# Kernel tuning notes

Hardware: AMD Instinct MI355X
Metric: run time of the kernel (lower is better)

## Reference

```python
import jax, jax.numpy as jnp
import numpy as np

N, IN_F, OUT_F = 8192, 512, 256
NEG_INF = -9e15
LEAKY_SLOPE = 0.25


def setup_inputs() -> dict:
    key = jax.random.key(0)
    k1, k2, k3, k4, k5, k6 = jax.random.split(key, 6)
    inp = {
        "input": jax.random.normal(k1, (N, IN_F), dtype=jnp.float32),
        "adj": jax.random.randint(k2, (N, N), 0, 2, dtype=jnp.int32),
        # learned params (xavier-normal-ish scale)
        "weights": jax.random.normal(k3, (IN_F, OUT_F), dtype=jnp.float32) * (2.0 / (IN_F + OUT_F)) ** 0.5,
        "a1": jax.random.normal(k4, (OUT_F, 1), dtype=jnp.float32) * (2.0 / (OUT_F + 1)) ** 0.5,
        "a2": jax.random.normal(k5, (OUT_F, 1), dtype=jnp.float32) * (2.0 / (OUT_F + 1)) ** 0.5,
        "bias": jax.random.uniform(k6, (OUT_F,), dtype=jnp.float32, minval=-1.0 / OUT_F ** 0.5, maxval=1.0 / OUT_F ** 0.5),
    }
    return inp


def reference(input, adj, weights, a1, a2, bias):
    # h = input @ W  : [N, out]
    h = input @ weights
    # e[i,j] = leaky_relu((h@a1)[i] + (h@a2)[j])  : [N, N] via broadcast
    e1 = h @ a1  # [N,1]
    e2 = h @ a2  # [N,1]
    e = e1 + e2.T
    e = jnp.where(e > 0, e, LEAKY_SLOPE * e)
    # mask non-edges, row softmax (dropout omitted: deterministic reference)
    scores = jnp.where(adj > 0, e, NEG_INF)
    attention = jax.nn.softmax(scores, axis=1)
    # aggregate + bias
    return attention @ h + bias
```

## Files before the change

### kernel.cpp

```cpp
#include <hip/hip_runtime.h>
#include <hip/hip_fp16.h>

typedef __attribute__((ext_vector_type(8))) short short8;
typedef __attribute__((ext_vector_type(4))) float floatx4;
typedef __attribute__((ext_vector_type(4))) unsigned int uintx4;
typedef __attribute__((ext_vector_type(2))) unsigned int uintx2;
typedef __attribute__((ext_vector_type(4))) int intx4;
typedef __attribute__((ext_vector_type(4))) unsigned short ushortx4;
typedef unsigned int u32;

#define NN 8192
#define KIN 512
#define COUT 256
#define SHIFT 16.0f

__device__ __forceinline__ unsigned int f2bf(float f) {
  unsigned int u = __float_as_uint(f);
  return (u + 0x7FFFu + ((u >> 16) & 1u)) >> 16;
}

__device__ __forceinline__ u32 pkbf(float lo, float hi) {
  u32 a = __float_as_uint(lo) + 0x8000u;
  u32 b = __float_as_uint(hi) + 0x8000u;
  return __builtin_amdgcn_perm(b, a, 0x07060302u);
}

__device__ __forceinline__ short8 pack8(const float* p) {
  uintx4 w;
  w.x = pkbf(p[0], p[1]);
  w.y = pkbf(p[2], p[3]);
  w.z = pkbf(p[4], p[5]);
  w.w = pkbf(p[6], p[7]);
  union { uintx4 u; short8 s; } cv; cv.u = w;
  return cv.s;
}

__global__ __launch_bounds__(256)
void k_prep(const float* __restrict__ in, ushortx4* __restrict__ inA4,
            const float* __restrict__ w, unsigned short* __restrict__ wt) {
  int b = blockIdx.x;
  if (b < 4096) {
    int idx = b * 256 + threadIdx.x;
    floatx4 v = ((const floatx4*)in)[idx];
    ushortx4 o;
    o.x = (unsigned short)f2bf(v.x);
    o.y = (unsigned short)f2bf(v.y);
    o.z = (unsigned short)f2bf(v.z);
    o.w = (unsigned short)f2bf(v.w);
    inA4[idx] = o;
  } else {
    int idx = (b - 4096) * 256 + threadIdx.x;
    int k = idx >> 8, c = idx & 255;
    wt[c * KIN + k] = (unsigned short)f2bf(w[idx]);
  }
}

__global__ __launch_bounds__(256)
void k_gemm_h(const unsigned short* __restrict__ inA, const unsigned short* __restrict__ wt,
              const float* __restrict__ a1, const float* __restrict__ a2,
              unsigned short* __restrict__ ht, float* __restrict__ e1, float* __restrict__ e2,
              float* __restrict__ A1, float* __restrict__ A2, u32* __restrict__ e2pk) {
  int wave = threadIdx.x >> 6;
  int lane = threadIdx.x & 63;
  int n = lane & 15, q = lane >> 4;
  int row0 = blockIdx.x * 64 + wave * 16;
  int mrow = row0 + n;

  floatx4 acc[16];
#pragma unroll
  for (int t = 0; t < 16; ++t) acc[t] = (floatx4){0.f, 0.f, 0.f, 0.f};

  for (int kc = 0; kc < KIN / 32; ++kc) {
    int k0 = kc * 32 + q * 8;
    short8 a = *(const short8*)(inA + (size_t)mrow * KIN + k0);
#pragma unroll
    for (int nt = 0; nt < 16; ++nt) {
      short8 b = *(const short8*)(wt + (size_t)(nt * 16 + n) * KIN + k0);
      acc[nt] = __builtin_amdgcn_mfma_f32_16x16x32_bf16(a, b, acc[nt], 0, 0, 0);
    }
  }

  int i0 = row0 + q * 4;
#pragma unroll
  for (int nt = 0; nt < 16; ++nt) {
    int c = nt * 16 + n;
    uintx2 pk;
    pk.x = f2bf(acc[nt][0]) | (f2bf(acc[nt][1]) << 16);
    pk.y = f2bf(acc[nt][2]) | (f2bf(acc[nt][3]) << 16);
    *(uintx2*)(ht + (size_t)c * NN + i0) = pk;
  }

  float s1[4] = {0.f, 0.f, 0.f, 0.f}, s2[4] = {0.f, 0.f, 0.f, 0.f};
#pragma unroll
  for (int nt = 0; nt < 16; ++nt) {
    float w1 = a1[nt * 16 + n];
    float w2 = a2[nt * 16 + n];
#pragma unroll
    for (int r = 0; r < 4; ++r) {
      s1[r] += acc[nt][r] * w1;
      s2[r] += acc[nt][r] * w2;
    }
  }
#pragma unroll
  for (int m = 1; m < 16; m <<= 1) {
#pragma unroll
    for (int r = 0; r < 4; ++r) {
      s1[r] += __shfl_xor(s1[r], m);
      s2[r] += __shfl_xor(s2[r], m);
    }
  }
  if (n == 0) {
#pragma unroll
    for (int r = 0; r < 4; ++r) {
      float v1 = s1[r], v2 = s2[r];
      e1[i0 + r] = v1;
      e2[i0 + r] = v2;
      A1[i0 + r] = __expf(v1 - 8.0f);
      A2[i0 + r] = __expf(0.25f * v1 - 8.0f);
      u32 b1 = f2bf(__expf(v2 - 8.0f));
      u32 b2 = f2bf(__expf(0.25f * v2 - 8.0f));
      e2pk[i0 + r] = (b1 << 16) | b2;
    }
  }
}

__global__ __launch_bounds__(256, 2)
void k_attn_direct(const int* __restrict__ adj, const unsigned short* __restrict__ ht,
                   const float* __restrict__ A1, const float* __restrict__ A2,
                   const u32* __restrict__ e2pk,
                   __half2* __restrict__ oph, float* __restrict__ Dpart) {
  int b = blockIdx.x;
  int rg = b >> 3, js = b & 7;
  int wave = threadIdx.x >> 6, lane = threadIdx.x & 63;
  int n = lane & 15, q = lane >> 4;
  int rowbase = rg * 128 + wave * 32;
  int jbeg = js * 1024;

  float A1v0 = A1[rowbase + n],      A2v0 = A2[rowbase + n];
  float A1v1 = A1[rowbase + 16 + n], A2v1 = A2[rowbase + 16 + n];

  floatx4 acc[2][16];
  floatx4 accd[2];
#pragma unroll
  for (int t = 0; t < 2; ++t) {
    accd[t] = (floatx4){0.f, 0.f, 0.f, 0.f};
#pragma unroll
    for (int nt = 0; nt < 16; ++nt) acc[t][nt] = (floatx4){0.f, 0.f, 0.f, 0.f};
  }

  union { uintx4 u; short8 s; } onesu;
  onesu.u = (uintx4){0x3F803F80u, 0x3F803F80u, 0x3F803F80u, 0x3F803F80u};
  short8 ones = onesu.s;

  const int* ar0 = adj + (size_t)(rowbase + n) * NN + jbeg + q * 8;
  const int* ar1 = adj + (size_t)(rowbase + 16 + n) * NN + jbeg + q * 8;
  const u32* ep  = e2pk + jbeg + q * 8;
  const unsigned short* hb = ht + (size_t)n * NN + jbeg + q * 8;

  for (int ch = 0; ch < 32; ++ch) {
    int jo = ch * 32;

    intx4 A00 = *(const intx4*)(ar0 + jo);
    intx4 A01 = *(const intx4*)(ar0 + jo + 4);
    intx4 A10 = *(const intx4*)(ar1 + jo);
    intx4 A11 = *(const intx4*)(ar1 + jo + 4);
    uintx4 ba = *(const uintx4*)(ep + jo);
    uintx4 bb = *(const uintx4*)(ep + jo + 4);
    u32 bw[8] = {ba.x, ba.y, ba.z, ba.w, bb.x, bb.y, bb.z, bb.w};

    float p0[8], p1[8];
#pragma unroll
    for (int jj = 0; jj < 8; ++jj) {
      int av0 = (jj < 4) ? A00[jj] : A01[jj - 4];
      int av1 = (jj < 4) ? A10[jj] : A11[jj - 4];
      float B1 = __uint_as_float(bw[jj] & 0xffff0000u);
      float B2 = __uint_as_float(bw[jj] << 16);
      float m10 = A1v0 * B1, m20 = A2v0 * B2;
      float m11 = A1v1 * B1, m21 = A2v1 * B2;
      float pm0 = fmaxf(m10, m20);
      float pm1 = fmaxf(m11, m21);
      p0[jj] = (av0 != 0) ? pm0 : 0.f;
      p1[jj] = (av1 != 0) ? pm1 : 0.f;
    }
    short8 af0 = pack8(p0);
    short8 af1 = pack8(p1);

#pragma unroll
    for (int t = 0; t < 16; ++t) {
      short8 bfv = *(const short8*)(hb + (size_t)(t * 16) * NN + jo);
      acc[0][t] = __builtin_amdgcn_mfma_f32_16x16x32_bf16(af0, bfv, acc[0][t], 0, 0, 0);
      acc[1][t] = __builtin_amdgcn_mfma_f32_16x16x32_bf16(af1, bfv, acc[1][t], 0, 0, 0);
    }
    accd[0] = __builtin_amdgcn_mfma_f32_16x16x32_bf16(af0, ones, accd[0], 0, 0, 0);
    accd[1] = __builtin_amdgcn_mfma_f32_16x16x32_bf16(af1, ones, accd[1], 0, 0, 0);
  }

  if (n == 0) {
#pragma unroll
    for (int t2 = 0; t2 < 2; ++t2)
#pragma unroll
      for (int r = 0; r < 4; ++r)
        Dpart[(size_t)js * NN + rowbase + t2 * 16 + q * 4 + r] = accd[t2][r];
  }

#pragma unroll
  for (int t2 = 0; t2 < 2; ++t2) {
    int ibase = rowbase + t2 * 16 + q * 4;
#pragma unroll
    for (int nt = 0; nt < 16; ++nt) {
      int c = nt * 16 + n;
      oph[((size_t)js * 4096 + (ibase >> 1)) * 256 + c] =
          __floats2half2_rn(acc[t2][nt][0], acc[t2][nt][1]);
      oph[((size_t)js * 4096 + (ibase >> 1) + 1) * 256 + c] =
          __floats2half2_rn(acc[t2][nt][2], acc[t2][nt][3]);
    }
  }
}

__global__ void k_final_part(float* __restrict__ out, const __half2* __restrict__ oph,
                             const float* __restrict__ Dpart, const float* __restrict__ bias) {
  int i = blockIdx.x;
  int c = threadIdx.x;
  int hi = i & 1;
  float s = 0.f, d = 0.f;
#pragma unroll
  for (int js = 0; js < 8; ++js) {
    __half2 h2 = oph[((size_t)js * 4096 + (i >> 1)) * 256 + c];
    s += hi ? __high2float(h2) : __low2float(h2);
    d += Dpart[(size_t)js * NN + i];
  }
  out[(size_t)i * COUT + c] = s / fmaxf(d, 1e-37f) + bias[c];
}

__global__ __launch_bounds__(256, 2)
void k_attn_atomic(const int* __restrict__ adj, const unsigned short* __restrict__ ht,
                   const float* __restrict__ e1, const float* __restrict__ e2,
                   float* __restrict__ out_num, float* __restrict__ Dbuf) {
  int b = blockIdx.x;
  int rg = b >> 3, js = b & 7;
  int wave = threadIdx.x >> 6, lane = threadIdx.x & 63;
  int n = lane & 15, q = lane >> 4;
  int rowbase = rg * 128 + wave * 32;

  float e1v0 = e1[rowbase + n];
  float e1v1 = e1[rowbase + 16 + n];

  floatx4 acc[2][16];
#pragma unroll
  for (int t = 0; t < 2; ++t)
#pragma unroll
    for (int nt = 0; nt < 16; ++nt) acc[t][nt] = (floatx4){0.f, 0.f, 0.f, 0.f};

  float d0 = 0.f, d1 = 0.f;
  int jbeg = js * 1024;

  for (int ch = 0; ch < 32; ++ch) {
    int j0 = jbeg + ch * 32 + q * 8;
    floatx4 ea = *(const floatx4*)(e2 + j0);
    floatx4 eb = *(const floatx4*)(e2 + j0 + 4);
    float ev[8] = {ea.x, ea.y, ea.z, ea.w, eb.x, eb.y, eb.z, eb.w};

    intx4 A00 = *(const intx4*)(adj + (size_t)(rowbase + n) * NN + j0);
    intx4 A01 = *(const intx4*)(adj + (size_t)(rowbase + n) * NN + j0 + 4);
    intx4 A10 = *(const intx4*)(adj + (size_t)(rowbase + 16 + n) * NN + j0);
    intx4 A11 = *(const intx4*)(adj + (size_t)(rowbase + 16 + n) * NN + j0 + 4);

    float p0[8], p1[8];
#pragma unroll
    for (int jj = 0; jj < 8; ++jj) {
      int av0 = (jj < 4) ? A00[jj] : A01[jj - 4];
      int av1 = (jj < 4) ? A10[jj] : A11[jj - 4];
      float t0 = e1v0 + ev[jj];
      float t1 = e1v1 + ev[jj];
      float f0 = fmaxf(t0, 0.25f * t0);
      float f1 = fmaxf(t1, 0.25f * t1);
      float x0 = __expf(f0 - SHIFT);
      float x1 = __expf(f1 - SHIFT);
      p0[jj] = (av0 != 0) ? x0 : 0.f;
      p1[jj] = (av1 != 0) ? x1 : 0.f;
      d0 += p0[jj];
      d1 += p1[jj];
    }
    short8 af0 = pack8(p0);
    short8 af1 = pack8(p1);

#pragma unroll
    for (int g = 0; g < 2; ++g) {
      short8 bf[8];
#pragma unroll
      for (int t = 0; t < 8; ++t)
        bf[t] = *(const short8*)(ht + (size_t)((g * 8 + t) * 16 + n) * NN + j0);
#pragma unroll
      for (int t = 0; t < 8; ++t) {
        acc[0][g * 8 + t] = __builtin_amdgcn_mfma_f32_16x16x32_bf16(af0, bf[t], acc[0][g * 8 + t], 0, 0, 0);
        acc[1][g * 8 + t] = __builtin_amdgcn_mfma_f32_16x16x32_bf16(af1, bf[t], acc[1][g * 8 + t], 0, 0, 0);
      }
    }
  }

  d0 += __shfl_xor(d0, 16); d0 += __shfl_xor(d0, 32);
  d1 += __shfl_xor(d1, 16); d1 += __shfl_xor(d1, 32);
  if (lane < 16) {
    atomicAdd(Dbuf + rowbase + lane, d0);
    atomicAdd(Dbuf + rowbase + 16 + lane, d1);
  }

#pragma unroll
  for (int t2 = 0; t2 < 2; ++t2) {
#pragma unroll
    for (int nt = 0; nt < 16; ++nt) {
#pragma unroll
      for (int r = 0; r < 4; ++r) {
        int i = rowbase + t2 * 16 + q * 4 + r;
        atomicAdd(out_num + (size_t)i * COUT + nt * 16 + n, acc[t2][nt][r]);
      }
    }
  }
}

__global__ void k_final_atomic(float* __restrict__ out, const float* __restrict__ Dbuf,
                               const float* __restrict__ bias) {
  int idx = blockIdx.x * 256 + threadIdx.x;
  int i = idx >> 8, c = idx & 255;
  float d = fmaxf(Dbuf[i], 1e-37f);
  out[idx] = out[idx] / d + bias[c];
}

extern "C" void kernel_launch(void* const* d_in, const int* in_sizes, int n_in,
                              void* d_out, int out_size, void* d_ws, size_t ws_size,
                              hipStream_t stream) {
  const float* input   = (const float*)d_in[0];
  const int*   adj     = (const int*)d_in[1];
  const float* weights = (const float*)d_in[2];
  const float* a1      = (const float*)d_in[3];
  const float* a2      = (const float*)d_in[4];
  const float* bias    = (const float*)d_in[5];
  float* out = (float*)d_out;
  char* ws = (char*)d_ws;

  unsigned short* inA = (unsigned short*)(ws);
  unsigned short* wt  = (unsigned short*)(ws + 8388608);
  unsigned short* ht  = (unsigned short*)(ws + 8650752);
  float* e1    = (float*)(ws + 12845056);
  float* e2    = (float*)(ws + 12877824);
  float* A1    = (float*)(ws + 12910592);
  float* A2    = (float*)(ws + 12943360);
  u32*   e2pk  = (u32*)  (ws + 12976128);
  float* Dpart = (float*)(ws + 13008896);
  __half2* oph = (__half2*)(ws + 13271040);
  const size_t WS_NEEDED_PART = 13271040 + (size_t)8 * NN * COUT * 2;
  float* Dbuf = Dpart;

  k_prep<<<4608, 256, 0, stream>>>(input, (ushortx4*)inA, weights, wt);
  k_gemm_h<<<128, 256, 0, stream>>>(inA, wt, a1, a2, ht, e1, e2, A1, A2, e2pk);

  if (ws_size >= WS_NEEDED_PART) {
    k_attn_direct<<<512, 256, 0, stream>>>(adj, ht, A1, A2, e2pk, oph, Dpart);
    k_final_part<<<8192, 256, 0, stream>>>(out, oph, Dpart, bias);
  } else {
    hipMemsetAsync(out, 0, (size_t)NN * COUT * sizeof(float), stream);
    hipMemsetAsync(Dbuf, 0, NN * sizeof(float), stream);
    k_attn_atomic<<<512, 256, 0, stream>>>(adj, ht, e1, e2, out, Dbuf);
    k_final_atomic<<<8192, 256, 0, stream>>>(out, Dbuf, bias);
  }
}
```

Baseline: 508.4 us.

## Stage h tiles through LDS with double-buffered async loads in attention kernel

The attention kernel now copies each 32-column chunk of the transposed h matrix into shared memory with global_load_lds, using an XOR-swizzled layout and two buffers. The copy for the next chunk and the register prefetch of the next adjacency values are issued before the current chunk is computed, and e2pk is loaded into LDS once per block. All four waves now share one h tile from LDS instead of each reading it from global memory, and memory latency overlaps with the MFMA work. The cost is 36 KB of LDS per block, two barriers per chunk, and hand-set vmcnt waits that must match the number of outstanding loads.

```diff
diff --git a/kernel.cpp b/kernel.cpp
--- a/kernel.cpp
+++ b/kernel.cpp
@@ -13,6 +13,13 @@
 #define KIN 512
 #define COUT 256
 #define SHIFT 16.0f
+
+#define AS1 __attribute__((address_space(1)))
+#define AS3 __attribute__((address_space(3)))
+
+__device__ __forceinline__ void stage16(const void* g, void* l) {
+  __builtin_amdgcn_global_load_lds((const AS1 u32*)g, (AS3 u32*)l, 16, 0, 0);
+}
 
 __device__ __forceinline__ unsigned int f2bf(float f) {
   unsigned int u = __float_as_uint(f);
@@ -125,16 +132,20 @@
 }
 
 __global__ __launch_bounds__(256, 2)
-void k_attn_direct(const int* __restrict__ adj, const unsigned short* __restrict__ ht,
-                   const float* __restrict__ A1, const float* __restrict__ A2,
-                   const u32* __restrict__ e2pk,
-                   __half2* __restrict__ oph, float* __restrict__ Dpart) {
+void k_attn_v3(const int* __restrict__ adj, const unsigned short* __restrict__ ht,
+               const float* __restrict__ A1, const float* __restrict__ A2,
+               const u32* __restrict__ e2pk,
+               __half2* __restrict__ oph, float* __restrict__ Dpart) {
+  __shared__ __align__(16) char smem[36864];
+  u32* e2s = (u32*)(smem + 32768);
+
   int b = blockIdx.x;
   int rg = b >> 3, js = b & 7;
   int wave = threadIdx.x >> 6, lane = threadIdx.x & 63;
   int n = lane & 15, q = lane >> 4;
   int rowbase = rg * 128 + wave * 32;
   int jbeg = js * 1024;
+  int swz = q ^ ((n >> 1) & 3);
 
   float A1v0 = A1[rowbase + n],      A2v0 = A2[rowbase + n];
   float A1v1 = A1[rowbase + 16 + n], A2v1 = A2[rowbase + 16 + n];
@@ -154,25 +165,50 @@
 
   const int* ar0 = adj + (size_t)(rowbase + n) * NN + jbeg + q * 8;
   const int* ar1 = adj + (size_t)(rowbase + 16 + n) * NN + jbeg + q * 8;
-  const u32* ep  = e2pk + jbeg + q * 8;
-  const unsigned short* hb = ht + (size_t)n * NN + jbeg + q * 8;
-
-  for (int ch = 0; ch < 32; ++ch) {
-    int jo = ch * 32;
-
-    intx4 A00 = *(const intx4*)(ar0 + jo);
-    intx4 A01 = *(const intx4*)(ar0 + jo + 4);
-    intx4 A10 = *(const intx4*)(ar1 + jo);
-    intx4 A11 = *(const intx4*)(ar1 + jo + 4);
-    uintx4 ba = *(const uintx4*)(ep + jo);
-    uintx4 bb = *(const uintx4*)(ep + jo + 4);
+
+  auto stage = [&](int ch, int buf) {
+    int j0g = jbeg + ch * 32;
+    char* hbase = smem + buf * 16384;
+#pragma unroll
+    for (int i = 0; i < 4; ++i) {
+      int seg = wave * 256 + i * 64 + lane;
+      int c = seg >> 2;
+      int o = (seg & 3) ^ ((seg >> 3) & 3);
+      stage16(ht + (size_t)c * NN + j0g + o * 8, hbase + (size_t)(wave * 256 + i * 64) * 16);
+    }
+  };
+
+  intx4 aA[4], aB[4];
+
+  stage(0, 0);
+  aA[0] = *(const intx4*)(ar0);
+  aA[1] = *(const intx4*)(ar0 + 4);
+  aA[2] = *(const intx4*)(ar1);
+  aA[3] = *(const intx4*)(ar1 + 4);
+  ((uintx4*)e2s)[threadIdx.x] = *(const uintx4*)(e2pk + jbeg + threadIdx.x * 4);
+  asm volatile("s_waitcnt lgkmcnt(0)" ::: "memory");
+  asm volatile("s_barrier" ::: "memory");
+
+  auto body = [&](int ch, intx4* aC, intx4* aN) {
+    int cur = ch & 1;
+    if (ch < 31) {
+      stage(ch + 1, cur ^ 1);
+      int jn = (ch + 1) * 32;
+      aN[0] = *(const intx4*)(ar0 + jn);
+      aN[1] = *(const intx4*)(ar0 + jn + 4);
+      aN[2] = *(const intx4*)(ar1 + jn);
+      aN[3] = *(const intx4*)(ar1 + jn + 4);
+    }
+
+    uintx4 ba = *(const uintx4*)(e2s + ch * 32 + q * 8);
+    uintx4 bb = *(const uintx4*)(e2s + ch * 32 + q * 8 + 4);
     u32 bw[8] = {ba.x, ba.y, ba.z, ba.w, bb.x, bb.y, bb.z, bb.w};
 
     float p0[8], p1[8];
 #pragma unroll
     for (int jj = 0; jj < 8; ++jj) {
-      int av0 = (jj < 4) ? A00[jj] : A01[jj - 4];
-      int av1 = (jj < 4) ? A10[jj] : A11[jj - 4];
+      int av0 = (jj < 4) ? aC[0][jj] : aC[1][jj - 4];
+      int av1 = (jj < 4) ? aC[2][jj] : aC[3][jj - 4];
       float B1 = __uint_as_float(bw[jj] & 0xffff0000u);
       float B2 = __uint_as_float(bw[jj] << 16);
       float m10 = A1v0 * B1, m20 = A2v0 * B2;
@@ -185,14 +221,30 @@
     short8 af0 = pack8(p0);
     short8 af1 = pack8(p1);
 
+    if (ch < 31) {
+      asm volatile("s_waitcnt vmcnt(8)" ::: "memory");
+    } else {
+      asm volatile("s_waitcnt vmcnt(0)" ::: "memory");
+    }
+    asm volatile("s_barrier" ::: "memory");
+
+    const short8* lb = (const short8*)(smem + (size_t)cur * 16384);
 #pragma unroll
     for (int t = 0; t < 16; ++t) {
-      short8 bfv = *(const short8*)(hb + (size_t)(t * 16) * NN + jo);
+      short8 bfv = lb[t * 64 + n * 4 + swz];
       acc[0][t] = __builtin_amdgcn_mfma_f32_16x16x32_bf16(af0, bfv, acc[0][t], 0, 0, 0);
       acc[1][t] = __builtin_amdgcn_mfma_f32_16x16x32_bf16(af1, bfv, acc[1][t], 0, 0, 0);
     }
     accd[0] = __builtin_amdgcn_mfma_f32_16x16x32_bf16(af0, ones, accd[0], 0, 0, 0);
     accd[1] = __builtin_amdgcn_mfma_f32_16x16x32_bf16(af1, ones, accd[1], 0, 0, 0);
+
+    asm volatile("s_waitcnt lgkmcnt(0)" ::: "memory");
+    asm volatile("s_barrier" ::: "memory");
+  };
+
+  for (int ch = 0; ch < 32; ch += 2) {
+    body(ch, aA, aB);
+    body(ch + 1, aB, aA);
   }
 
   if (n == 0) {
@@ -355,7 +407,7 @@
   k_gemm_h<<<128, 256, 0, stream>>>(inA, wt, a1, a2, ht, e1, e2, A1, A2, e2pk);
 
   if (ws_size >= WS_NEEDED_PART) {
-    k_attn_direct<<<512, 256, 0, stream>>>(adj, ht, A1, A2, e2pk, oph, Dpart);
+    k_attn_v3<<<512, 256, 0, stream>>>(adj, ht, A1, A2, e2pk, oph, Dpart);
     k_final_part<<<8192, 256, 0, stream>>>(out, oph, Dpart, bias);
   } else {
     hipMemsetAsync(out, 0, (size_t)NN * COUT * sizeof(float), stream);
```

Result: faster. 454.4 us (-10.6%).

## Stage h tiles into LDS via async global_load_lds with 4-deep pipeline

Applied to the files above, without the earlier changes.

The attention kernel becomes 512-thread blocks with 8 waves of 16 rows each. Each block cooperatively stages the shared ht column tile into XOR-swizzled LDS with global_load_lds, using a 4-buffer ring and prefetching two chunks ahead. The e2 packed values go to LDS and adjacency loads are double-buffered in registers. Previously every wave loaded h straight from global memory, so this removes that redundant traffic at the cost of roughly 132KB of LDS per block and a barrier per chunk. The h GEMM also moves to 128-thread blocks with twice as many blocks.

```diff
diff --git a/kernel.cpp b/kernel.cpp
--- a/kernel.cpp
+++ b/kernel.cpp
@@ -13,6 +13,13 @@
 #define KIN 512
 #define COUT 256
 #define SHIFT 16.0f
+
+#define AS1 __attribute__((address_space(1)))
+#define AS3 __attribute__((address_space(3)))
+
+__device__ __forceinline__ void stage16(const void* g, void* l) {
+  __builtin_amdgcn_global_load_lds((const AS1 u32*)g, (AS3 u32*)l, 16, 0, 0);
+}
 
 __device__ __forceinline__ unsigned int f2bf(float f) {
   unsigned int u = __float_as_uint(f);
@@ -55,7 +62,7 @@
   }
 }
 
-__global__ __launch_bounds__(256)
+__global__ __launch_bounds__(128)
 void k_gemm_h(const unsigned short* __restrict__ inA, const unsigned short* __restrict__ wt,
               const float* __restrict__ a1, const float* __restrict__ a2,
               unsigned short* __restrict__ ht, float* __restrict__ e1, float* __restrict__ e2,
@@ -63,7 +70,7 @@
   int wave = threadIdx.x >> 6;
   int lane = threadIdx.x & 63;
   int n = lane & 15, q = lane >> 4;
-  int row0 = blockIdx.x * 64 + wave * 16;
+  int row0 = blockIdx.x * 32 + wave * 16;
   int mrow = row0 + n;
 
   floatx4 acc[16];
@@ -124,96 +131,133 @@
   }
 }
 
-__global__ __launch_bounds__(256, 2)
-void k_attn_direct(const int* __restrict__ adj, const unsigned short* __restrict__ ht,
-                   const float* __restrict__ A1, const float* __restrict__ A2,
-                   const u32* __restrict__ e2pk,
-                   __half2* __restrict__ oph, float* __restrict__ Dpart) {
+__global__ __launch_bounds__(512, 2)
+void k_attn_v7(const int* __restrict__ adj, const unsigned short* __restrict__ ht,
+               const float* __restrict__ A1, const float* __restrict__ A2,
+               const u32* __restrict__ e2pk,
+               __half2* __restrict__ oph, float* __restrict__ Dpart) {
+  __shared__ __align__(16) char smem[135168];
+  u32* e2s = (u32*)(smem + 131072);
+
   int b = blockIdx.x;
   int rg = b >> 3, js = b & 7;
   int wave = threadIdx.x >> 6, lane = threadIdx.x & 63;
   int n = lane & 15, q = lane >> 4;
-  int rowbase = rg * 128 + wave * 32;
+  int rowbase = rg * 128 + wave * 16;
   int jbeg = js * 1024;
 
-  float A1v0 = A1[rowbase + n],      A2v0 = A2[rowbase + n];
-  float A1v1 = A1[rowbase + 16 + n], A2v1 = A2[rowbase + 16 + n];
-
-  floatx4 acc[2][16];
-  floatx4 accd[2];
-#pragma unroll
-  for (int t = 0; t < 2; ++t) {
-    accd[t] = (floatx4){0.f, 0.f, 0.f, 0.f};
-#pragma unroll
-    for (int nt = 0; nt < 16; ++nt) acc[t][nt] = (floatx4){0.f, 0.f, 0.f, 0.f};
-  }
+  float A1v = A1[rowbase + n], A2v = A2[rowbase + n];
+
+  floatx4 acc[16];
+  floatx4 accd = (floatx4){0.f, 0.f, 0.f, 0.f};
+#pragma unroll
+  for (int t = 0; t < 16; ++t) acc[t] = (floatx4){0.f, 0.f, 0.f, 0.f};
 
   union { uintx4 u; short8 s; } onesu;
   onesu.u = (uintx4){0x3F803F80u, 0x3F803F80u, 0x3F803F80u, 0x3F803F80u};
   short8 ones = onesu.s;
 
-  const int* ar0 = adj + (size_t)(rowbase + n) * NN + jbeg + q * 8;
-  const int* ar1 = adj + (size_t)(rowbase + 16 + n) * NN + jbeg + q * 8;
-  const u32* ep  = e2pk + jbeg + q * 8;
-  const unsigned short* hb = ht + (size_t)n * NN + jbeg + q * 8;
-
-  for (int ch = 0; ch < 32; ++ch) {
-    int jo = ch * 32;
-
-    intx4 A00 = *(const intx4*)(ar0 + jo);
-    intx4 A01 = *(const intx4*)(ar0 + jo + 4);
-    intx4 A10 = *(const intx4*)(ar1 + jo);
-    intx4 A11 = *(const intx4*)(ar1 + jo + 4);
-    uintx4 ba = *(const uintx4*)(ep + jo);
-    uintx4 bb = *(const uintx4*)(ep + jo + 4);
-    u32 bw[8] = {ba.x, ba.y, ba.z, ba.w, bb.x, bb.y, bb.z, bb.w};
-
-    float p0[8], p1[8];
-#pragma unroll
-    for (int jj = 0; jj < 8; ++jj) {
-      int av0 = (jj < 4) ? A00[jj] : A01[jj - 4];
-      int av1 = (jj < 4) ? A10[jj] : A11[jj - 4];
-      float B1 = __uint_as_float(bw[jj] & 0xffff0000u);
-      float B2 = __uint_as_float(bw[jj] << 16);
-      float m10 = A1v0 * B1, m20 = A2v0 * B2;
-      float m11 = A1v1 * B1, m21 = A2v1 * B2;
-      float pm0 = fmaxf(m10, m20);
-      float pm1 = fmaxf(m11, m21);
-      p0[jj] = (av0 != 0) ? pm0 : 0.f;
-      p1[jj] = (av1 != 0) ? pm1 : 0.f;
-    }
-    short8 af0 = pack8(p0);
-    short8 af1 = pack8(p1);
-
+  const int* ar = adj + (size_t)(rowbase + n) * NN + jbeg + q * 8;
+
+  auto stage = [&](int ch, int buf) {
+    int j0g = jbeg + ch * 64;
+    char* hbase = smem + buf * 32768;
+#pragma unroll
+    for (int i = 0; i < 4; ++i) {
+      int seg = wave * 256 + i * 64 + lane;
+      int row = seg >> 3;
+      int o = (seg & 7) ^ (row & 7);
+      stage16(ht + (size_t)row * NN + j0g + o * 8,
+              hbase + (size_t)(wave * 256 + i * 64) * 16);
+    }
+  };
+
+  auto ldadj = [&](int ch, intx4* A) {
+    const int* p = ar + ch * 64;
+    A[0] = *(const intx4*)(p);
+    A[1] = *(const intx4*)(p + 4);
+    A[2] = *(const intx4*)(p + 32);
+    A[3] = *(const intx4*)(p + 36);
+  };
+
+  intx4 aA[4], aB[4];
+
+  uintx2 ev = *(const uintx2*)(e2pk + jbeg + threadIdx.x * 2);
+  ((uintx2*)e2s)[threadIdx.x] = ev;
+  asm volatile("" ::: "memory");
+  stage(0, 0);
+  ldadj(0, aA);
+  stage(1, 1);
+  ldadj(1, aB);
+  asm volatile("s_waitcnt lgkmcnt(0)" ::: "memory");
+  asm volatile("s_barrier" ::: "memory");
+
+  auto body = [&](int ch, intx4* aC, int wcnt, bool doPf) {
+    if (doPf) stage(ch + 2, (ch + 2) & 3);
+
+    short8 af0, af1;
+#pragma unroll
+    for (int h = 0; h < 2; ++h) {
+      uintx4 ba = *(const uintx4*)(e2s + ch * 64 + h * 32 + q * 8);
+      uintx4 bb = *(const uintx4*)(e2s + ch * 64 + h * 32 + q * 8 + 4);
+      u32 bw[8] = {ba.x, ba.y, ba.z, ba.w, bb.x, bb.y, bb.z, bb.w};
+      intx4 w0 = (h == 0) ? aC[0] : aC[2];
+      intx4 w1 = (h == 0) ? aC[1] : aC[3];
+      float p0[8];
+#pragma unroll
+      for (int jj = 0; jj < 8; ++jj) {
+        int av = (jj < 4) ? w0[jj] : w1[jj - 4];
+        float B1 = __uint_as_float(bw[jj] & 0xffff0000u);
+        float B2 = __uint_as_float(bw[jj] << 16);
+        float pm = fmaxf(A1v * B1, A2v * B2);
+        p0[jj] = (av != 0) ? pm : 0.f;
+      }
+      if (h == 0) af0 = pack8(p0); else af1 = pack8(p0);
+    }
+
+    if (doPf) ldadj(ch + 2, aC);
+
+    if (wcnt == 16)     asm volatile("s_waitcnt vmcnt(16)" ::: "memory");
+    else if (wcnt == 8) asm volatile("s_waitcnt vmcnt(8)" ::: "memory");
+    else                asm volatile("s_waitcnt vmcnt(0)" ::: "memory");
+    asm volatile("s_barrier" ::: "memory");
+
+    const short8* lb = (const short8*)(smem + (size_t)(ch & 3) * 32768);
 #pragma unroll
     for (int t = 0; t < 16; ++t) {
-      short8 bfv = *(const short8*)(hb + (size_t)(t * 16) * NN + jo);
-      acc[0][t] = __builtin_amdgcn_mfma_f32_16x16x32_bf16(af0, bfv, acc[0][t], 0, 0, 0);
-      acc[1][t] = __builtin_amdgcn_mfma_f32_16x16x32_bf16(af1, bfv, acc[1][t], 0, 0, 0);
-    }
-    accd[0] = __builtin_amdgcn_mfma_f32_16x16x32_bf16(af0, ones, accd[0], 0, 0, 0);
-    accd[1] = __builtin_amdgcn_mfma_f32_16x16x32_bf16(af1, ones, accd[1], 0, 0, 0);
-  }
+      short8 bfv = lb[(t * 16 + n) * 8 + ((q) ^ (n & 7))];
+      acc[t] = __builtin_amdgcn_mfma_f32_16x16x32_bf16(af0, bfv, acc[t], 0, 0, 0);
+    }
+    accd = __builtin_amdgcn_mfma_f32_16x16x32_bf16(af0, ones, accd, 0, 0, 0);
+#pragma unroll
+    for (int t = 0; t < 16; ++t) {
+      short8 bfv = lb[(t * 16 + n) * 8 + ((4 + q) ^ (n & 7))];
+      acc[t] = __builtin_amdgcn_mfma_f32_16x16x32_bf16(af1, bfv, acc[t], 0, 0, 0);
+    }
+    accd = __builtin_amdgcn_mfma_f32_16x16x32_bf16(af1, ones, accd, 0, 0, 0);
+  };
+
+  for (int c2 = 0; c2 < 14; c2 += 2) {
+    body(c2, aA, 16, true);
+    body(c2 + 1, aB, 16, true);
+  }
+  body(14, aA, 8, false);
+  body(15, aB, 0, false);
 
   if (n == 0) {
 #pragma unroll
-    for (int t2 = 0; t2 < 2; ++t2)
-#pragma unroll
-      for (int r = 0; r < 4; ++r)
-        Dpart[(size_t)js * NN + rowbase + t2 * 16 + q * 4 + r] = accd[t2][r];
-  }
-
-#pragma unroll
-  for (int t2 = 0; t2 < 2; ++t2) {
-    int ibase = rowbase + t2 * 16 + q * 4;
-#pragma unroll
-    for (int nt = 0; nt < 16; ++nt) {
-      int c = nt * 16 + n;
-      oph[((size_t)js * 4096 + (ibase >> 1)) * 256 + c] =
-          __floats2half2_rn(acc[t2][nt][0], acc[t2][nt][1]);
-      oph[((size_t)js * 4096 + (ibase >> 1) + 1) * 256 + c] =
-          __floats2half2_rn(acc[t2][nt][2], acc[t2][nt][3]);
-    }
+    for (int r = 0; r < 4; ++r)
+      Dpart[(size_t)js * NN + rowbase + q * 4 + r] = accd[r];
+  }
+
+  int ibase = rowbase + q * 4;
+#pragma unroll
+  for (int t = 0; t < 16; ++t) {
+    int c = t * 16 + n;
+    oph[((size_t)js * 4096 + (ibase >> 1)) * 256 + c] =
+        __floats2half2_rn(acc[t][0], acc[t][1]);
+    oph[((size_t)js * 4096 + (ibase >> 1) + 1) * 256 + c] =
+        __floats2half2_rn(acc[t][2], acc[t][3]);
   }
 }
 
@@ -352,10 +396,10 @@
   float* Dbuf = Dpart;
 
   k_prep<<<4608, 256, 0, stream>>>(input, (ushortx4*)inA, weights, wt);
-  k_gemm_h<<<128, 256, 0, stream>>>(inA, wt, a1, a2, ht, e1, e2, A1, A2, e2pk);
+  k_gemm_h<<<256, 128, 0, stream>>>(inA, wt, a1, a2, ht, e1, e2, A1, A2, e2pk);
 
   if (ws_size >= WS_NEEDED_PART) {
-    k_attn_direct<<<512, 256, 0, stream>>>(adj, ht, A1, A2, e2pk, oph, Dpart);
+    k_attn_v7<<<512, 512, 0, stream>>>(adj, ht, A1, A2, e2pk, oph, Dpart);
     k_final_part<<<8192, 256, 0, stream>>>(out, oph, Dpart, bias);
   } else {
     hipMemsetAsync(out, 0, (size_t)NN * COUT * sizeof(float), stream);
```

Measured after the change: 437.2 us. 1.16x faster.
